# Optimization experiments

Hardware: AMD Instinct MI355X
Metric: run time of the kernel (lower is better)

Reference implementation:

```python
import jax, jax.numpy as jnp
import numpy as np

NC = 151  # number of object classes (VG)
NR = 51   # number of relation classes (VG)


def setup_inputs() -> dict:
    key = jax.random.key(0)
    ks = jax.random.split(key, 10)
    B, N, D = 32, 100, 4096
    H = D // 4
    w = lambda k, shape, fan_in: (jax.random.normal(k, shape, jnp.float32) / np.sqrt(fan_in).astype(np.float32))
    return {
        "encoder_reps": jax.random.normal(ks[0], (B * N, D), jnp.float32),
        "W_comp": w(ks[1], (D, H), D),        # obj_comp Linear (no bias)
        "W_ou1": w(ks[2], (H, H), H),         # ou1 Linear
        "W_ofc": w(ks[3], (H, H), H),         # ofc_u Linear
        "W_decomp": w(ks[4], (H, D), H),      # obj_decomp Linear
        "conv1": w(ks[5], (10, NR, 3, 3), NR * 9),  # Conv2d(51,10,3,pad=1)
        "conv2": w(ks[6], (5, 10, 3, 3), 10 * 9),   # Conv2d(10,5,3,pad=1)
        "conv3": w(ks[7], (1, 5, 1, 1), 5),         # Conv2d(5,1,1)
        "freq_emb": jax.random.normal(ks[8], (NC * NC, NR), jnp.float32) * 0.01,
        "obj_preds": jax.random.randint(ks[9], (B * N,), 0, NC),
        "num_obj": 100,
    }


def reference(encoder_reps, W_comp, W_ou1, W_ofc, W_decomp, conv1, conv2, conv3, freq_emb, obj_preds, num_obj):
    T, D = encoder_reps.shape
    N = num_obj
    B = T // N
    relu = jax.nn.relu
    # obj_comp then per-image ou1 (vectorized over images)
    comp = relu(encoder_reps @ W_comp).reshape(B, N, -1)   # [B,N,H]
    obj_u1 = relu(comp @ W_ou1)                             # [B,N,H]
    # product-index frequency-bias gather: emb[subj*NC + obj]
    labels = obj_preds.reshape(B, N)
    pair_idx = labels[:, :, None] * NC + labels[:, None, :]  # [B,N,N]
    adj_fg = freq_emb[pair_idx]                               # [B,N,N,NR]
    # adjacency net: Conv-Conv-Conv-Tanh over the NxN 'image' with NR channels
    x = jnp.transpose(adj_fg, (0, 3, 1, 2))                   # [B,NR,N,N]
    dn = ("NCHW", "OIHW", "NCHW")
    x = jax.lax.conv_general_dilated(x, conv1, (1, 1), "SAME", dimension_numbers=dn)
    x = jax.lax.conv_general_dilated(x, conv2, (1, 1), "SAME", dimension_numbers=dn)
    x = jnp.tanh(jax.lax.conv_general_dilated(x, conv3, (1, 1), "SAME", dimension_numbers=dn))
    adj = x[:, 0]                                             # [B,N,N]
    # graph message passing: adj @ obj_u1, then ofc_u / decomp + residual
    ofl_u = jnp.einsum("bnm,bmh->bnh", adj, obj_u1).reshape(T, -1)
    u_m = relu(ofl_u @ W_ofc)
    decomp = relu(u_m @ W_decomp)
    return decomp + encoder_reps
```

## Files before the change

### kernel.cpp

```cpp
#include <hip/hip_runtime.h>
#include <cmath>

#define NCC 151
#define NRCH 51
#define BDIM 32
#define NOBJ 100
#define DDIM 4096
#define HDIM 1024
#define TDIM (BDIM * NOBJ)

typedef __bf16 bf16_t;
typedef __bf16 bf16x8 __attribute__((ext_vector_type(8)));
typedef __bf16 bf16x4 __attribute__((ext_vector_type(4)));
typedef float f32x4 __attribute__((ext_vector_type(4)));

template <bool RELU, bool ADDF32OUT, int SPLITK>
__global__ __launch_bounds__(256) void gemm_bf16(
    const bf16_t* __restrict__ A,
    const bf16_t* __restrict__ Bt,
    const float* __restrict__ add,
    void* __restrict__ Cout,
    int N, int K, size_t MN) {
  __shared__ __align__(16) bf16_t Asm[128 * 64];
  __shared__ __align__(16) bf16_t Bsm[128 * 64];
  const int tid = threadIdx.x;
  const int lane = tid & 63;
  const int w = tid >> 6;
  const int wm = w >> 1, wn = w & 1;

  const int nx = gridDim.x, ny = gridDim.y;
  int lin = blockIdx.x + nx * (blockIdx.y + ny * blockIdx.z);
  const int nwg = nx * ny * gridDim.z;
  const int q = nwg >> 3;
  lin = (lin & 7) * q + (lin >> 3);
  const int bx = lin % nx;
  const int r2 = lin / nx;
  const int by = r2 % ny;
  const int bz = r2 / ny;

  const int bm = by * 128, bn = bx * 128;
  const int lr = lane & 15;
  const int lk = lane >> 4;

  int kBeg = 0, kEnd = K;
  if (SPLITK > 1) {
    const int chunk = (((K / 64) + SPLITK - 1) / SPLITK) * 64;
    kBeg = bz * chunk;
    kEnd = min(K, kBeg + chunk);
  }

  f32x4 acc[4][4];
#pragma unroll
  for (int m = 0; m < 4; ++m)
#pragma unroll
    for (int n = 0; n < 4; ++n) acc[m][n] = (f32x4){0.f, 0.f, 0.f, 0.f};

  const int srow = tid >> 3;
  const int sslot = tid & 7;

  char* ldsA = (char*)Asm;
  char* ldsB = (char*)Bsm;

  for (int kt = kBeg; kt < kEnd; kt += 64) {
    __syncthreads();
#pragma unroll
    for (int i = 0; i < 4; ++i) {
      const int row = i * 32 + srow;
      const int kc = sslot ^ (row & 7);
      const bf16_t* ga = A + (size_t)(bm + row) * K + kt + kc * 8;
      const bf16_t* gb = Bt + (size_t)(bn + row) * K + kt + kc * 8;
      __builtin_amdgcn_global_load_lds(
          (const __attribute__((address_space(1))) void*)ga,
          (__attribute__((address_space(3))) void*)(ldsA + i * 4096 + w * 1024),
          16, 0, 0);
      __builtin_amdgcn_global_load_lds(
          (const __attribute__((address_space(1))) void*)gb,
          (__attribute__((address_space(3))) void*)(ldsB + i * 4096 + w * 1024),
          16, 0, 0);
    }
    __syncthreads();

    bf16x8 af[4][2], bfr[4][2];
#pragma unroll
    for (int m = 0; m < 4; ++m) {
      const int row = wm * 64 + m * 16 + lr;
#pragma unroll
      for (int kk = 0; kk < 2; ++kk) {
        const int slot = kk * 4 + lk;
        af[m][kk] =
            *(const bf16x8*)(ldsA + row * 128 + ((slot ^ (lr & 7)) << 4));
      }
    }
#pragma unroll
    for (int n = 0; n < 4; ++n) {
      const int row = wn * 64 + n * 16 + lr;
#pragma unroll
      for (int kk = 0; kk < 2; ++kk) {
        const int slot = kk * 4 + lk;
        bfr[n][kk] =
            *(const bf16x8*)(ldsB + row * 128 + ((slot ^ (lr & 7)) << 4));
      }
    }
#pragma unroll
    for (int m = 0; m < 4; ++m)
#pragma unroll
      for (int n = 0; n < 4; ++n) {
        acc[m][n] = __builtin_amdgcn_mfma_f32_16x16x32_bf16(
            af[m][0], bfr[n][0], acc[m][n], 0, 0, 0);
        acc[m][n] = __builtin_amdgcn_mfma_f32_16x16x32_bf16(
            af[m][1], bfr[n][1], acc[m][n], 0, 0, 0);
      }
  }

  const int or0 = bm + wm * 64 + lk * 4;
  const int oc0 = bn + wn * 64 + lr;
#pragma unroll
  for (int m = 0; m < 4; ++m)
#pragma unroll
    for (int n = 0; n < 4; ++n)
#pragma unroll
      for (int r = 0; r < 4; ++r) {
        float v = acc[m][n][r];
        const size_t off = (size_t)(or0 + m * 16 + r) * N + (oc0 + n * 16);
        if (SPLITK > 1) {
          ((float*)Cout)[bz * MN + off] = v;
        } else {
          if (RELU) v = fmaxf(v, 0.f);
          if (ADDF32OUT)
            ((float*)Cout)[off] = v + add[off];
          else
            ((bf16_t*)Cout)[off] = (bf16_t)v;
        }
      }
}

__global__ __launch_bounds__(256) void reduce3_kernel(
    const float* __restrict__ p, bf16_t* __restrict__ out, int n4) {
  int i = blockIdx.x * 256 + threadIdx.x;
  if (i >= n4) return;
  const f32x4* pv = (const f32x4*)p;
  f32x4 v = pv[i] + pv[i + n4] + pv[i + 2 * (size_t)n4];
  bf16x4 o = {(bf16_t)fmaxf(v[0], 0.f), (bf16_t)fmaxf(v[1], 0.f),
              (bf16_t)fmaxf(v[2], 0.f), (bf16_t)fmaxf(v[3], 0.f)};
  ((bf16x4*)out)[i] = o;
}

__global__ __launch_bounds__(256) void cvt_bf16_kernel(
    const float* __restrict__ in, bf16_t* __restrict__ out, int n4) {
  int i = blockIdx.x * 256 + threadIdx.x;
  if (i >= n4) return;
  float4 v = ((const float4*)in)[i];
  bf16x4 o = {(bf16_t)v.x, (bf16_t)v.y, (bf16_t)v.z, (bf16_t)v.w};
  ((bf16x4*)out)[i] = o;
}

__global__ __launch_bounds__(256) void transT_kernel(
    const float* __restrict__ in, bf16_t* __restrict__ out, int K, int N) {
  __shared__ float t[32][33];
  const int n0 = blockIdx.x * 32, k0 = blockIdx.y * 32;
  const int tx = threadIdx.x & 31, ty = threadIdx.x >> 5;
#pragma unroll
  for (int i = 0; i < 4; ++i)
    t[ty + i * 8][tx] = in[(size_t)(k0 + ty + i * 8) * N + n0 + tx];
  __syncthreads();
#pragma unroll
  for (int i = 0; i < 4; ++i)
    out[(size_t)(n0 + ty + i * 8) * K + k0 + tx] = (bf16_t)t[tx][ty + i * 8];
}

__global__ __launch_bounds__(256) void prep_w1r_kernel(
    const float* __restrict__ w1, float* __restrict__ w1r) {
  int idx = blockIdx.x * 256 + threadIdx.x;
  if (idx >= NRCH * 90) return;
  int ci = idx / 90, r = idx % 90, k9 = r / 10, co = r % 10;
  w1r[idx] = w1[((co * NRCH + ci) * 3 + k9 / 3) * 3 + (k9 % 3)];
}

__global__ __launch_bounds__(128) void prep_w23_kernel(
    const float* __restrict__ w2, const float* __restrict__ w3,
    float* __restrict__ w23) {
  int t = threadIdx.x;
  if (t >= 90) return;
  int k9 = t / 10, c2 = t % 10;
  float acc = 0.f;
#pragma unroll
  for (int c3 = 0; c3 < 5; ++c3)
    acc += w3[c3] * w2[((c3 * 10 + c2) * 3 + k9 / 3) * 3 + (k9 % 3)];
  w23[t] = acc;
}

__global__ __launch_bounds__(256) void pidx_kernel(
    const int* __restrict__ preds, int* __restrict__ pidx) {
  int idx = blockIdx.x * 256 + threadIdx.x;
  if (idx >= BDIM * NOBJ * NOBJ) return;
  int j = idx % NOBJ;
  int i = (idx / NOBJ) % NOBJ;
  int b = idx / (NOBJ * NOBJ);
  pidx[idx] = preds[b * NOBJ + i] * NCC + preds[b * NOBJ + j];
}

__global__ __launch_bounds__(128) void femb1_kernel(
    const float* __restrict__ femb, const float* __restrict__ w1r,
    float* __restrict__ femb1) {
  __shared__ float row[NRCH];
  const int p = blockIdx.x;
  if (threadIdx.x < NRCH)
    row[threadIdx.x] = femb[(size_t)p * NRCH + threadIdx.x];
  __syncthreads();
  const int t = threadIdx.x;
  if (t >= 90) return;
  float acc = 0.f;
#pragma unroll
  for (int ci = 0; ci < NRCH; ++ci) acc += row[ci] * w1r[ci * 90 + t];
  femb1[((size_t)p * 9 + t / 10) * 12 + (t % 10)] = acc;
}

__global__ __launch_bounds__(256) void conv1g_kernel(
    const int* __restrict__ pidx, const float* __restrict__ femb1,
    float* __restrict__ x1) {
  int idx = blockIdx.x * 256 + threadIdx.x;
  if (idx >= BDIM * NOBJ * NOBJ) return;
  int j = idx % NOBJ;
  int i = (idx / NOBJ) % NOBJ;
  int b = idx / (NOBJ * NOBJ);
  f32x4 a0 = {0.f, 0.f, 0.f, 0.f}, a1 = a0, a2 = a0;
  const int* pb = pidx + b * NOBJ * NOBJ;
#pragma unroll
  for (int kh = 0; kh < 3; ++kh) {
    int ii = i + kh - 1;
    if (ii < 0 || ii >= NOBJ) continue;
#pragma unroll
    for (int kw = 0; kw < 3; ++kw) {
      int jj = j + kw - 1;
      if (jj < 0 || jj >= NOBJ) continue;
      int p = pb[ii * NOBJ + jj];
      const f32x4* f =
          (const f32x4*)(femb1 + ((size_t)p * 9 + kh * 3 + kw) * 12);
      a0 += f[0];
      a1 += f[1];
      a2 += f[2];
    }
  }
  f32x4* o = (f32x4*)(x1 + (size_t)idx * 12);
  o[0] = a0;
  o[1] = a1;
  o[2] = a2;
}

__global__ __launch_bounds__(256) void conv23_kernel(
    const float* __restrict__ x1, const float* __restrict__ w23,
    float* __restrict__ adj) {
  __shared__ float w[90];
  if (threadIdx.x < 90) w[threadIdx.x] = w23[threadIdx.x];
  __syncthreads();
  int idx = blockIdx.x * 256 + threadIdx.x;
  if (idx >= BDIM * NOBJ * NOBJ) return;
  int j = idx % NOBJ;
  int i = (idx / NOBJ) % NOBJ;
  int b = idx / (NOBJ * NOBJ);
  float acc = 0.f;
  const float* xb = x1 + (size_t)b * NOBJ * NOBJ * 12;
#pragma unroll
  for (int kh = 0; kh < 3; ++kh) {
    int ii = i + kh - 1;
    if (ii < 0 || ii >= NOBJ) continue;
#pragma unroll
    for (int kw = 0; kw < 3; ++kw) {
      int jj = j + kw - 1;
      if (jj < 0 || jj >= NOBJ) continue;
      const float* xr = xb + (ii * NOBJ + jj) * 12;
      const float* wr = w + (kh * 3 + kw) * 10;
#pragma unroll
      for (int c = 0; c < 10; ++c) acc += wr[c] * xr[c];
    }
  }
  adj[idx] = tanhf(acc);
}

__global__ __launch_bounds__(256) void einsum_kernel(
    const float* __restrict__ adj, const bf16_t* __restrict__ u1,
    bf16_t* __restrict__ out) {
  int b = blockIdx.x / NOBJ;
  int n = blockIdx.x % NOBJ;
  __shared__ float arow[NOBJ];
  if (threadIdx.x < NOBJ)
    arow[threadIdx.x] = adj[((size_t)b * NOBJ + n) * NOBJ + threadIdx.x];
  __syncthreads();
  const bf16_t* ub = u1 + (size_t)b * NOBJ * HDIM;
  const int h0 = threadIdx.x * 4;
  float a0 = 0.f, a1 = 0.f, a2 = 0.f, a3 = 0.f;
  for (int m = 0; m < NOBJ; ++m) {
    float a = arow[m];
    bf16x4 v = *(const bf16x4*)(ub + (size_t)m * HDIM + h0);
    a0 += a * (float)v[0];
    a1 += a * (float)v[1];
    a2 += a * (float)v[2];
    a3 += a * (float)v[3];
  }
  bf16x4 o = {(bf16_t)a0, (bf16_t)a1, (bf16_t)a2, (bf16_t)a3};
  *(bf16x4*)(out + ((size_t)b * NOBJ + n) * HDIM + h0) = o;
}

extern "C" void kernel_launch(void* const* d_in, const int* in_sizes, int n_in,
                              void* d_out, int out_size, void* d_ws,
                              size_t ws_size, hipStream_t stream) {
  const float* enc = (const float*)d_in[0];
  const float* W_comp = (const float*)d_in[1];
  const float* W_ou1 = (const float*)d_in[2];
  const float* W_ofc = (const float*)d_in[3];
  const float* W_dec = (const float*)d_in[4];
  const float* conv1w = (const float*)d_in[5];
  const float* conv2w = (const float*)d_in[6];
  const float* conv3w = (const float*)d_in[7];
  const float* femb = (const float*)d_in[8];
  const int* preds = (const int*)d_in[9];
  float* out = (float*)d_out;
  char* wsb = (char*)d_ws;

  const size_t MN = (size_t)TDIM * HDIM;

  bf16_t* encb   = (bf16_t*)(wsb + 0);
  bf16_t* WcompT = (bf16_t*)(wsb + 26214400);
  bf16_t* comp   = (bf16_t*)(wsb + 34603008);
  float*  part3  = (float*)(wsb + 41156608);
  bf16_t* Wou1T  = (bf16_t*)(wsb + 41156608);
  float*  w1r    = (float*)(wsb + 43253760);
  float*  w23    = (float*)(wsb + 43272128);
  float*  femb1  = (float*)(wsb + 43272512);
  int*    pidx   = (int*)(wsb + 53122560);
  float*  x1     = (float*)(wsb + 54402560);
  bf16_t* obj_u1 = (bf16_t*)(wsb + 69762560);
  float*  adj    = (float*)(wsb + 76316160);
  bf16_t* ofl_u  = (bf16_t*)(wsb + 0);
  bf16_t* WofcT  = (bf16_t*)(wsb + 6553600);
  bf16_t* u_m    = (bf16_t*)(wsb + 8650752);
  bf16_t* WdecT  = (bf16_t*)(wsb + 15204352);

  cvt_bf16_kernel<<<(TDIM * DDIM / 4 + 255) / 256, 256, 0, stream>>>(
      enc, encb, TDIM * DDIM / 4);
  transT_kernel<<<dim3(HDIM / 32, DDIM / 32), 256, 0, stream>>>(
      W_comp, WcompT, DDIM, HDIM);

  gemm_bf16<false, false, 3>
      <<<dim3(HDIM / 128, TDIM / 128, 3), 256, 0, stream>>>(
          encb, WcompT, nullptr, part3, HDIM, DDIM, MN);
  reduce3_kernel<<<(int)(MN / 4 / 256), 256, 0, stream>>>(part3, comp,
                                                          (int)(MN / 4));

  transT_kernel<<<dim3(HDIM / 32, HDIM / 32), 256, 0, stream>>>(
      W_ou1, Wou1T, HDIM, HDIM);
  gemm_bf16<true, false, 1>
      <<<dim3(HDIM / 128, TDIM / 128), 256, 0, stream>>>(
          comp, Wou1T, nullptr, obj_u1, HDIM, HDIM, MN);

  prep_w1r_kernel<<<(NRCH * 90 + 255) / 256, 256, 0, stream>>>(conv1w, w1r);
  prep_w23_kernel<<<1, 128, 0, stream>>>(conv2w, conv3w, w23);
  pidx_kernel<<<(BDIM * NOBJ * NOBJ + 255) / 256, 256, 0, stream>>>(preds,
                                                                    pidx);
  femb1_kernel<<<NCC * NCC, 128, 0, stream>>>(femb, w1r, femb1);

  conv1g_kernel<<<(BDIM * NOBJ * NOBJ + 255) / 256, 256, 0, stream>>>(
      pidx, femb1, x1);
  conv23_kernel<<<(BDIM * NOBJ * NOBJ + 255) / 256, 256, 0, stream>>>(x1, w23,
                                                                      adj);

  transT_kernel<<<dim3(HDIM / 32, HDIM / 32), 256, 0, stream>>>(
      W_ofc, WofcT, HDIM, HDIM);
  transT_kernel<<<dim3(DDIM / 32, HDIM / 32), 256, 0, stream>>>(
      W_dec, WdecT, HDIM, DDIM);

  einsum_kernel<<<BDIM * NOBJ, 256, 0, stream>>>(adj, obj_u1, ofl_u);

  gemm_bf16<true, false, 1>
      <<<dim3(HDIM / 128, TDIM / 128), 256, 0, stream>>>(
          ofl_u, WofcT, nullptr, u_m, HDIM, HDIM, MN);
  gemm_bf16<true, true, 1>
      <<<dim3(DDIM / 128, TDIM / 128), 256, 0, stream>>>(
          u_m, WdecT, enc, out, DDIM, HDIM, MN);
}
```

Baseline: 289.4 us.

## Use MFMA for adjacency einsum and bf16 six-way split-K for obj_comp

The scalar per-row einsum kernel is replaced by an MFMA kernel. It stages each batch's 100x100 adjacency and the u1 tile in swizzled LDS, zero-padded to K=128, and computes 128x128 output tiles. The first GEMM's split-K rises from 3 to 6 to fill more CUs, and its partials are stored as bf16 so the reduction traffic stays the same. The costs are extra rounding from the bf16 partials, wasted MFMA work on the padding, and a scattered transpose store into LDS.

```diff
diff --git a/kernel.cpp b/kernel.cpp
--- a/kernel.cpp
+++ b/kernel.cpp
@@ -123,7 +123,7 @@
         float v = acc[m][n][r];
         const size_t off = (size_t)(or0 + m * 16 + r) * N + (oc0 + n * 16);
         if (SPLITK > 1) {
-          ((float*)Cout)[bz * MN + off] = v;
+          ((bf16_t*)Cout)[bz * MN + off] = (bf16_t)v;
         } else {
           if (RELU) v = fmaxf(v, 0.f);
           if (ADDF32OUT)
@@ -134,15 +134,22 @@
       }
 }
 
-__global__ __launch_bounds__(256) void reduce3_kernel(
-    const float* __restrict__ p, bf16_t* __restrict__ out, int n4) {
+__global__ __launch_bounds__(256) void reduce6_kernel(
+    const bf16_t* __restrict__ p, bf16_t* __restrict__ out, int n8,
+    size_t MN) {
   int i = blockIdx.x * 256 + threadIdx.x;
-  if (i >= n4) return;
-  const f32x4* pv = (const f32x4*)p;
-  f32x4 v = pv[i] + pv[i + n4] + pv[i + 2 * (size_t)n4];
-  bf16x4 o = {(bf16_t)fmaxf(v[0], 0.f), (bf16_t)fmaxf(v[1], 0.f),
-              (bf16_t)fmaxf(v[2], 0.f), (bf16_t)fmaxf(v[3], 0.f)};
-  ((bf16x4*)out)[i] = o;
+  if (i >= n8) return;
+  float s[8] = {};
+#pragma unroll
+  for (int z = 0; z < 6; ++z) {
+    bf16x8 v = *(const bf16x8*)(p + z * MN + (size_t)i * 8);
+#pragma unroll
+    for (int j = 0; j < 8; ++j) s[j] += (float)v[j];
+  }
+  bf16x8 o;
+#pragma unroll
+  for (int j = 0; j < 8; ++j) o[j] = (bf16_t)fmaxf(s[j], 0.f);
+  *(bf16x8*)(out + (size_t)i * 8) = o;
 }
 
 __global__ __launch_bounds__(256) void cvt_bf16_kernel(
@@ -277,28 +284,101 @@
   adj[idx] = tanhf(acc);
 }
 
-__global__ __launch_bounds__(256) void einsum_kernel(
-    const float* __restrict__ adj, const bf16_t* __restrict__ u1,
-    bf16_t* __restrict__ out) {
-  int b = blockIdx.x / NOBJ;
-  int n = blockIdx.x % NOBJ;
-  __shared__ float arow[NOBJ];
-  if (threadIdx.x < NOBJ)
-    arow[threadIdx.x] = adj[((size_t)b * NOBJ + n) * NOBJ + threadIdx.x];
+__global__ __launch_bounds__(256) void einsum_mfma_kernel(
+    const float* __restrict__ adj,
+    const bf16_t* __restrict__ u1,
+    bf16_t* __restrict__ ofl) {
+  __shared__ __align__(16) bf16_t As[128 * 128];
+  __shared__ __align__(16) bf16_t Us[128 * 128];
+  const int b = blockIdx.y;
+  const int h0 = blockIdx.x * 128;
+  const int tid = threadIdx.x, lane = tid & 63, w = tid >> 6;
+  const int wm = w >> 1, wn = w & 1;
+  const int lr = lane & 15, lk = lane >> 4;
+
+  {
+    f32x4 z = {0.f, 0.f, 0.f, 0.f};
+#pragma unroll
+    for (int i = 0; i < 8; ++i) ((f32x4*)As)[tid + i * 256] = z;
+#pragma unroll
+    for (int i = 0; i < 8; ++i) ((f32x4*)Us)[tid + i * 256] = z;
+  }
   __syncthreads();
-  const bf16_t* ub = u1 + (size_t)b * NOBJ * HDIM;
-  const int h0 = threadIdx.x * 4;
-  float a0 = 0.f, a1 = 0.f, a2 = 0.f, a3 = 0.f;
-  for (int m = 0; m < NOBJ; ++m) {
-    float a = arow[m];
-    bf16x4 v = *(const bf16x4*)(ub + (size_t)m * HDIM + h0);
-    a0 += a * (float)v[0];
-    a1 += a * (float)v[1];
-    a2 += a * (float)v[2];
-    a3 += a * (float)v[3];
-  }
-  bf16x4 o = {(bf16_t)a0, (bf16_t)a1, (bf16_t)a2, (bf16_t)a3};
-  *(bf16x4*)(out + ((size_t)b * NOBJ + n) * HDIM + h0) = o;
+
+  const float* ab = adj + (size_t)b * 10000;
+#pragma unroll
+  for (int i = 0; i < 10; ++i) {
+    int idx = tid + i * 256;
+    if (idx < 2500) {
+      int row = idx / 25, kc = idx % 25;
+      f32x4 v = ((const f32x4*)ab)[idx];
+      bf16x4 o = {(bf16_t)v[0], (bf16_t)v[1], (bf16_t)v[2], (bf16_t)v[3]};
+      int slot = kc >> 1;
+      *(bf16x4*)((char*)As + row * 256 + ((slot ^ (row & 7)) << 4) +
+                 (kc & 1) * 8) = o;
+    }
+  }
+
+  const bf16_t* ub = u1 + (size_t)b * 100 * HDIM + h0;
+#pragma unroll
+  for (int i = 0; i < 7; ++i) {
+    int idx = tid + i * 256;
+    if (idx < 1600) {
+      int hc = idx / 100, m = idx % 100;
+      bf16x8 v = *(const bf16x8*)(ub + (size_t)m * HDIM + hc * 8);
+      int slot = m >> 3, mr = m & 7;
+#pragma unroll
+      for (int j = 0; j < 8; ++j) {
+        int h = hc * 8 + j;
+        *((bf16_t*)((char*)Us + h * 256 + ((slot ^ (h & 7)) << 4) + mr * 2)) =
+            v[j];
+      }
+    }
+  }
+  __syncthreads();
+
+  f32x4 acc[4][4];
+#pragma unroll
+  for (int m = 0; m < 4; ++m)
+#pragma unroll
+    for (int n = 0; n < 4; ++n) acc[m][n] = (f32x4){0.f, 0.f, 0.f, 0.f};
+
+#pragma unroll
+  for (int ks = 0; ks < 4; ++ks) {
+    bf16x8 a[4], u[4];
+#pragma unroll
+    for (int m = 0; m < 4; ++m) {
+      int row = wm * 64 + m * 16 + lr;
+      int slot = ks * 4 + lk;
+      a[m] = *(const bf16x8*)((char*)As + row * 256 + ((slot ^ (lr & 7)) << 4));
+    }
+#pragma unroll
+    for (int n = 0; n < 4; ++n) {
+      int row = wn * 64 + n * 16 + lr;
+      int slot = ks * 4 + lk;
+      u[n] = *(const bf16x8*)((char*)Us + row * 256 + ((slot ^ (lr & 7)) << 4));
+    }
+#pragma unroll
+    for (int m = 0; m < 4; ++m)
+#pragma unroll
+      for (int n = 0; n < 4; ++n)
+        acc[m][n] =
+            __builtin_amdgcn_mfma_f32_16x16x32_bf16(a[m], u[n], acc[m][n], 0, 0, 0);
+  }
+
+  const int or0 = wm * 64 + lk * 4;
+  const int oc0 = h0 + wn * 64 + lr;
+#pragma unroll
+  for (int m = 0; m < 4; ++m)
+#pragma unroll
+    for (int n = 0; n < 4; ++n)
+#pragma unroll
+      for (int r = 0; r < 4; ++r) {
+        int row = or0 + m * 16 + r;
+        if (row < 100)
+          ofl[((size_t)b * 100 + row) * HDIM + oc0 + n * 16] =
+              (bf16_t)acc[m][n][r];
+      }
 }
 
 extern "C" void kernel_launch(void* const* d_in, const int* in_sizes, int n_in,
@@ -322,7 +402,7 @@
   bf16_t* encb   = (bf16_t*)(wsb + 0);
   bf16_t* WcompT = (bf16_t*)(wsb + 26214400);
   bf16_t* comp   = (bf16_t*)(wsb + 34603008);
-  float*  part3  = (float*)(wsb + 41156608);
+  bf16_t* part6  = (bf16_t*)(wsb + 41156608);
   bf16_t* Wou1T  = (bf16_t*)(wsb + 41156608);
   float*  w1r    = (float*)(wsb + 43253760);
   float*  w23    = (float*)(wsb + 43272128);
@@ -341,11 +421,11 @@
   transT_kernel<<<dim3(HDIM / 32, DDIM / 32), 256, 0, stream>>>(
       W_comp, WcompT, DDIM, HDIM);
 
-  gemm_bf16<false, false, 3>
-      <<<dim3(HDIM / 128, TDIM / 128, 3), 256, 0, stream>>>(
-          encb, WcompT, nullptr, part3, HDIM, DDIM, MN);
-  reduce3_kernel<<<(int)(MN / 4 / 256), 256, 0, stream>>>(part3, comp,
-                                                          (int)(MN / 4));
+  gemm_bf16<false, false, 6>
+      <<<dim3(HDIM / 128, TDIM / 128, 6), 256, 0, stream>>>(
+          encb, WcompT, nullptr, part6, HDIM, DDIM, MN);
+  reduce6_kernel<<<(int)(MN / 8 / 256), 256, 0, stream>>>(part6, comp,
+                                                          (int)(MN / 8), MN);
 
   transT_kernel<<<dim3(HDIM / 32, HDIM / 32), 256, 0, stream>>>(
       W_ou1, Wou1T, HDIM, HDIM);
@@ -369,7 +449,8 @@
   transT_kernel<<<dim3(DDIM / 32, HDIM / 32), 256, 0, stream>>>(
       W_dec, WdecT, HDIM, DDIM);
 
-  einsum_kernel<<<BDIM * NOBJ, 256, 0, stream>>>(adj, obj_u1, ofl_u);
+  einsum_mfma_kernel<<<dim3(HDIM / 128, BDIM), 256, 0, stream>>>(adj, obj_u1,
+                                                                 ofl_u);
 
   gemm_bf16<true, false, 1>
       <<<dim3(HDIM / 128, TDIM / 128), 256, 0, stream>>>(
```

Result: faster. 244.0 us (-15.7%).
